# Optimization experiments

Hardware: AMD Instinct MI355X
Metric: run time of the kernel (lower is better)

## Reference

```python
import jax, jax.numpy as jnp
import numpy as np

N_GRAPHS = 8


def glorot(key, shape):
    fan_in, fan_out = shape[0], shape[1]
    s = (6.0 / (fan_in + fan_out)) ** 0.5
    return jax.random.uniform(key, shape, jnp.float32, -s, s)


def setup_inputs() -> dict:
    key = jax.random.key(0)
    ks = jax.random.split(key, 8)
    N, E, C = 100000, 800000, 128
    x = jax.random.normal(ks[0], (N, C), jnp.float32)
    edge_index = jax.random.randint(ks[1], (2, E), 0, N, jnp.int64)
    batch = jnp.sort(jax.random.randint(ks[2], (N,), 0, N_GRAPHS, jnp.int64))
    W1 = glorot(ks[3], (C, 64));   b1 = jnp.zeros((64,), jnp.float32)
    W2 = glorot(ks[4], (64, 128)); b2 = jnp.zeros((128,), jnp.float32)
    W3 = glorot(ks[5], (128, 256)); b3 = jnp.zeros((256,), jnp.float32)
    Wfc = glorot(ks[6], (256, 1))
    bfc = jax.random.normal(ks[7], (1,), jnp.float32) * 0.01
    return {"x": x, "edge_index": edge_index, "batch": batch,
            "W1": W1, "b1": b1, "W2": W2, "b2": b2, "W3": W3, "b3": b3,
            "Wfc": Wfc, "bfc": bfc}


def _gcn_layer(h_in, W, b, src, dst, norm_edge, self_coef, n):
    # GCNConv: x' = D^{-1/2}(A+I)D^{-1/2} (x W) + b   (self-loops included)
    h = h_in @ W                                     # [N, out]
    msg = h[src] * norm_edge[:, None]                # gather + edge normalize
    agg = jax.ops.segment_sum(msg, dst, num_segments=n)  # scatter-add
    agg = agg + h * self_coef[:, None]               # self-loop contribution
    return agg + b


def reference(x, edge_index, batch, W1, b1, W2, b2, W3, b3, Wfc, bfc):
    n = x.shape[0]
    src, dst = edge_index[0], edge_index[1]
    # gcn_norm with self-loops: deg = in-degree + 1
    deg = jax.ops.segment_sum(jnp.ones_like(dst, dtype=x.dtype), dst, num_segments=n) + 1.0
    dis = deg ** -0.5
    norm_edge = dis[src] * dis[dst]
    self_coef = dis * dis
    h = jax.nn.relu(_gcn_layer(x, W1, b1, src, dst, norm_edge, self_coef, n))
    h = jax.nn.relu(_gcn_layer(h, W2, b2, src, dst, norm_edge, self_coef, n))
    h = jax.nn.relu(_gcn_layer(h, W3, b3, src, dst, norm_edge, self_coef, n))
    # global_mean_pool over graphs
    counts = jax.ops.segment_sum(jnp.ones((n,), x.dtype), batch, num_segments=N_GRAPHS)
    pooled = jax.ops.segment_sum(h, batch, num_segments=N_GRAPHS) / counts[:, None]
    return pooled @ Wfc + bfc
```

## Files before the change

### kernel.cpp

```cpp
#include <hip/hip_runtime.h>
#include <hip/hip_bf16.h>

typedef __attribute__((ext_vector_type(8))) short short8v;
typedef __attribute__((ext_vector_type(4))) float f32x4;

static __device__ __forceinline__ unsigned short f2bf(float f) {
  __hip_bfloat16 b = __float2bfloat16(f);
  return *reinterpret_cast<unsigned short*>(&b);
}
static __device__ __forceinline__ float bf2f(unsigned short u) {
  unsigned int x = ((unsigned int)u) << 16;
  return __builtin_bit_cast(float, x);
}
static __device__ __forceinline__ float bflo(unsigned int u) {
  return __builtin_bit_cast(float, u << 16);
}
static __device__ __forceinline__ float bfhi(unsigned int u) {
  return __builtin_bit_cast(float, u & 0xffff0000u);
}

__global__ __launch_bounds__(256) void k_hist(const int* __restrict__ ei,
                                              int* __restrict__ cnt, int E) {
  int stride = gridDim.x * blockDim.x;
  for (int i = blockIdx.x * blockDim.x + threadIdx.x; i < E; i += stride)
    atomicAdd(&cnt[ei[E + i]], 1);
}

__global__ __launch_bounds__(256) void k_scan1(const int* __restrict__ cnt,
                                               int* __restrict__ row_tmp,
                                               int* __restrict__ bsum, int N) {
  __shared__ int sd[256];
  const int tid = threadIdx.x;
  const int i = blockIdx.x * 256 + tid;
  int v = (i < N) ? cnt[i] : 0;
  sd[tid] = v;
  __syncthreads();
#pragma unroll
  for (int off = 1; off < 256; off <<= 1) {
    int t = (tid >= off) ? sd[tid - off] : 0;
    __syncthreads();
    sd[tid] += t;
    __syncthreads();
  }
  if (i < N) row_tmp[i] = sd[tid] - v;
  if (tid == 255) bsum[blockIdx.x] = sd[255];
}

__global__ __launch_bounds__(1024) void k_scan2(int* __restrict__ bsum, int nb) {
  __shared__ int sd[1024];
  const int t = threadIdx.x;
  int v = (t < nb) ? bsum[t] : 0;
  sd[t] = v;
  __syncthreads();
#pragma unroll
  for (int off = 1; off < 1024; off <<= 1) {
    int x = (t >= off) ? sd[t - off] : 0;
    __syncthreads();
    sd[t] += x;
    __syncthreads();
  }
  if (t < nb) bsum[t] = sd[t] - v;
}

__global__ __launch_bounds__(256) void k_scan3(const int* __restrict__ row_tmp,
                                               const int* __restrict__ bsum,
                                               const int* __restrict__ cnt,
                                               const int* __restrict__ batch,
                                               float* __restrict__ dis,
                                               int* __restrict__ row_ptr,
                                               int* __restrict__ bucket_cur,
                                               int* __restrict__ gstart, int N,
                                               int E) {
  const int i = blockIdx.x * 256 + threadIdx.x;
  if (i < N) {
    int rp = row_tmp[i] + bsum[i >> 8];
    row_ptr[i] = rp;
    if ((i & 255) == 0) bucket_cur[i >> 8] = rp;
    dis[i] = 1.0f / sqrtf((float)cnt[i] + 1.0f);
    int b = batch[i];
    if (i == 0) {
      for (int g = 0; g <= b; ++g) gstart[g] = 0;
    } else {
      int p = batch[i - 1];
      for (int g = p + 1; g <= b; ++g) gstart[g] = i;
    }
    if (i == N - 1)
      for (int g = b + 1; g <= 8; ++g) gstart[g] = N;
  }
  if (i == 0) row_ptr[N] = E;
}

__global__ __launch_bounds__(256) void k_b3(const int* __restrict__ ei,
                                            int* __restrict__ bucket_cur,
                                            uint2* __restrict__ pairs, int E) {
  __shared__ int cntD[512];
  __shared__ int gbase[512];
  const int t = threadIdx.x;
  for (int i = t; i < 512; i += 256) cntD[i] = 0;
  __syncthreads();
  const int base = blockIdx.x * 2048;
  int s[8], d[8], rk[8];
#pragma unroll
  for (int i = 0; i < 8; ++i) {
    int e = base + i * 256 + t;
    if (e < E) {
      s[i] = ei[e];
      d[i] = ei[E + e];
      rk[i] = atomicAdd(&cntD[d[i] >> 8], 1);
    }
  }
  __syncthreads();
  for (int i = t; i < 512; i += 256)
    if (cntD[i] > 0) gbase[i] = atomicAdd(&bucket_cur[i], cntD[i]);
  __syncthreads();
#pragma unroll
  for (int i = 0; i < 8; ++i) {
    int e = base + i * 256 + t;
    if (e < E)
      pairs[gbase[d[i] >> 8] + rk[i]] = make_uint2((unsigned)s[i], (unsigned)d[i]);
  }
}

__global__ __launch_bounds__(256) void k_b4(const int* __restrict__ row_ptr,
                                            const uint2* __restrict__ pairs,
                                            int* __restrict__ col, int N) {
  __shared__ int curL[257];
  const int n0 = blockIdx.x << 8;
  const int nn = min(256, N - n0);
  const int t = threadIdx.x;
  for (int i = t; i <= nn; i += 256) curL[i] = row_ptr[n0 + i];
  __syncthreads();
  const int p0 = curL[0], p1 = curL[nn];
  __syncthreads();
  for (int idx = p0 + t; idx < p1; idx += 256) {
    uint2 pr = pairs[idx];
    int pos = atomicAdd(&curL[(int)pr.y - n0], 1);
    col[pos] = (int)pr.x;
  }
}

static __device__ __forceinline__ void pack_one(const float* __restrict__ W,
                                                unsigned short* __restrict__ Wp,
                                                int K, int M, int t) {
  int KT = K >> 5;
  int lane = t & 63;
  int tile = t >> 6;
  int kt = tile % KT;
  int ct = tile / KT;
  int c = ct * 16 + (lane & 15);
  int k0 = kt * 32 + (lane >> 4) * 8;
  unsigned short v[8];
#pragma unroll
  for (int j = 0; j < 8; ++j) v[j] = f2bf(W[(size_t)(k0 + j) * M + c]);
  ushort4* dst = (ushort4*)&Wp[(size_t)t * 8];
  dst[0] = make_ushort4(v[0], v[1], v[2], v[3]);
  dst[1] = make_ushort4(v[4], v[5], v[6], v[7]);
}

__global__ __launch_bounds__(256) void k_packall(
    const float* __restrict__ W1, const float* __restrict__ W2,
    const float* __restrict__ W3, unsigned short* __restrict__ Wp1,
    unsigned short* __restrict__ Wp2, unsigned short* __restrict__ Wp3) {
  int t = blockIdx.x * 256 + threadIdx.x;
  if (t < 1024)
    pack_one(W1, Wp1, 128, 64, t);
  else if (t < 2048)
    pack_one(W2, Wp2, 64, 128, t - 1024);
  else if (t < 6144)
    pack_one(W3, Wp3, 128, 256, t - 2048);
}

template <bool EPI>
__global__ __launch_bounds__(256) void k_agg64(const int* __restrict__ row_ptr,
                                               const int* __restrict__ col,
                                               const float* __restrict__ dis,
                                               const unsigned short* __restrict__ Hin,
                                               const float* __restrict__ bias,
                                               unsigned short* __restrict__ Pout,
                                               int N) {
  const int lane = threadIdx.x & 63;
  int d = blockIdx.x * 4 + (threadIdx.x >> 6);
  if (d >= N) return;
  const int q = lane >> 3;
  const int cl = lane & 7;
  const int cb = cl * 8;
  const float disd = dis[d];
  const int beg = row_ptr[d];
  const int end = row_ptr[d + 1];
  const int deg = end - beg;
  const int nedge = min(deg, 64);

  int s_l = d;
  float w_l = 0.f;
  if (lane < nedge) {
    s_l = col[beg + lane];
    w_l = dis[s_l] * disd;
  }

  float acc[8];
#pragma unroll
  for (int k = 0; k < 8; ++k) acc[k] = 0.f;
  if (q == 0) {
    uint4 u = *(const uint4*)&Hin[(size_t)d * 64 + cb];
    const float sc = disd * disd;
    acc[0] = bflo(u.x) * sc; acc[1] = bfhi(u.x) * sc;
    acc[2] = bflo(u.y) * sc; acc[3] = bfhi(u.y) * sc;
    acc[4] = bflo(u.z) * sc; acc[5] = bfhi(u.z) * sc;
    acc[6] = bflo(u.w) * sc; acc[7] = bfhi(u.w) * sc;
  }

  const int padded = (nedge + 15) & ~15;
  for (int base = 0; base < padded; base += 16) {
    int e0 = base + q, e1 = base + 8 + q;
    int s0 = __shfl(s_l, e0, 64);
    float w0 = __shfl(w_l, e0, 64);
    int s1 = __shfl(s_l, e1, 64);
    float w1 = __shfl(w_l, e1, 64);
    if (e0 >= nedge) { s0 = d; w0 = 0.f; }
    if (e1 >= nedge) { s1 = d; w1 = 0.f; }
    uint4 u0 = *(const uint4*)&Hin[(size_t)s0 * 64 + cb];
    uint4 u1 = *(const uint4*)&Hin[(size_t)s1 * 64 + cb];
    acc[0] = fmaf(bflo(u0.x), w0, acc[0]); acc[1] = fmaf(bfhi(u0.x), w0, acc[1]);
    acc[2] = fmaf(bflo(u0.y), w0, acc[2]); acc[3] = fmaf(bfhi(u0.y), w0, acc[3]);
    acc[4] = fmaf(bflo(u0.z), w0, acc[4]); acc[5] = fmaf(bfhi(u0.z), w0, acc[5]);
    acc[6] = fmaf(bflo(u0.w), w0, acc[6]); acc[7] = fmaf(bfhi(u0.w), w0, acc[7]);
    acc[0] = fmaf(bflo(u1.x), w1, acc[0]); acc[1] = fmaf(bfhi(u1.x), w1, acc[1]);
    acc[2] = fmaf(bflo(u1.y), w1, acc[2]); acc[3] = fmaf(bfhi(u1.y), w1, acc[3]);
    acc[4] = fmaf(bflo(u1.z), w1, acc[4]); acc[5] = fmaf(bfhi(u1.z), w1, acc[5]);
    acc[6] = fmaf(bflo(u1.w), w1, acc[6]); acc[7] = fmaf(bfhi(u1.w), w1, acc[7]);
  }
  if (deg > 64) {
    for (int j = beg + 64 + q; j < end; j += 8) {
      int s = col[j];
      float w = dis[s] * disd;
      uint4 u = *(const uint4*)&Hin[(size_t)s * 64 + cb];
      acc[0] = fmaf(bflo(u.x), w, acc[0]); acc[1] = fmaf(bfhi(u.x), w, acc[1]);
      acc[2] = fmaf(bflo(u.y), w, acc[2]); acc[3] = fmaf(bfhi(u.y), w, acc[3]);
      acc[4] = fmaf(bflo(u.z), w, acc[4]); acc[5] = fmaf(bfhi(u.z), w, acc[5]);
      acc[6] = fmaf(bflo(u.w), w, acc[6]); acc[7] = fmaf(bfhi(u.w), w, acc[7]);
    }
  }

#pragma unroll
  for (int k = 0; k < 8; ++k) {
    acc[k] += __shfl_xor(acc[k], 8, 64);
    acc[k] += __shfl_xor(acc[k], 16, 64);
    acc[k] += __shfl_xor(acc[k], 32, 64);
  }
  if (q == 0) {
    if (EPI) {
#pragma unroll
      for (int k = 0; k < 8; ++k) acc[k] = fmaxf(acc[k] + bias[cb + k], 0.f);
    }
    uint4 o;
    o.x = (unsigned)f2bf(acc[0]) | ((unsigned)f2bf(acc[1]) << 16);
    o.y = (unsigned)f2bf(acc[2]) | ((unsigned)f2bf(acc[3]) << 16);
    o.z = (unsigned)f2bf(acc[4]) | ((unsigned)f2bf(acc[5]) << 16);
    o.w = (unsigned)f2bf(acc[6]) | ((unsigned)f2bf(acc[7]) << 16);
    *(uint4*)&Pout[(size_t)d * 64 + cb] = o;
  }
}

__global__ __launch_bounds__(256) void k_agg128(const int* __restrict__ row_ptr,
                                                const int* __restrict__ col,
                                                const float* __restrict__ dis,
                                                const unsigned short* __restrict__ Hin,
                                                unsigned short* __restrict__ Pout,
                                                int N) {
  const int lane = threadIdx.x & 63;
  int d = blockIdx.x * 4 + (threadIdx.x >> 6);
  if (d >= N) return;
  const int q = lane >> 4;
  const int cl = lane & 15;
  const int cb = cl * 8;
  const float disd = dis[d];
  const int beg = row_ptr[d];
  const int end = row_ptr[d + 1];
  const int deg = end - beg;
  const int nedge = min(deg, 64);

  int s_l = d;
  float w_l = 0.f;
  if (lane < nedge) {
    s_l = col[beg + lane];
    w_l = dis[s_l] * disd;
  }

  float acc[8];
#pragma unroll
  for (int k = 0; k < 8; ++k) acc[k] = 0.f;
  if (q == 0) {
    uint4 u = *(const uint4*)&Hin[(size_t)d * 128 + cb];
    const float sc = disd * disd;
    acc[0] = bflo(u.x) * sc; acc[1] = bfhi(u.x) * sc;
    acc[2] = bflo(u.y) * sc; acc[3] = bfhi(u.y) * sc;
    acc[4] = bflo(u.z) * sc; acc[5] = bfhi(u.z) * sc;
    acc[6] = bflo(u.w) * sc; acc[7] = bfhi(u.w) * sc;
  }

  const int padded = (nedge + 7) & ~7;
  for (int base = 0; base < padded; base += 8) {
    int e0 = base + q, e1 = base + 4 + q;
    int s0 = __shfl(s_l, e0, 64);
    float w0 = __shfl(w_l, e0, 64);
    int s1 = __shfl(s_l, e1, 64);
    float w1 = __shfl(w_l, e1, 64);
    if (e0 >= nedge) { s0 = d; w0 = 0.f; }
    if (e1 >= nedge) { s1 = d; w1 = 0.f; }
    uint4 u0 = *(const uint4*)&Hin[(size_t)s0 * 128 + cb];
    uint4 u1 = *(const uint4*)&Hin[(size_t)s1 * 128 + cb];
    acc[0] = fmaf(bflo(u0.x), w0, acc[0]); acc[1] = fmaf(bfhi(u0.x), w0, acc[1]);
    acc[2] = fmaf(bflo(u0.y), w0, acc[2]); acc[3] = fmaf(bfhi(u0.y), w0, acc[3]);
    acc[4] = fmaf(bflo(u0.z), w0, acc[4]); acc[5] = fmaf(bfhi(u0.z), w0, acc[5]);
    acc[6] = fmaf(bflo(u0.w), w0, acc[6]); acc[7] = fmaf(bfhi(u0.w), w0, acc[7]);
    acc[0] = fmaf(bflo(u1.x), w1, acc[0]); acc[1] = fmaf(bfhi(u1.x), w1, acc[1]);
    acc[2] = fmaf(bflo(u1.y), w1, acc[2]); acc[3] = fmaf(bfhi(u1.y), w1, acc[3]);
    acc[4] = fmaf(bflo(u1.z), w1, acc[4]); acc[5] = fmaf(bfhi(u1.z), w1, acc[5]);
    acc[6] = fmaf(bflo(u1.w), w1, acc[6]); acc[7] = fmaf(bfhi(u1.w), w1, acc[7]);
  }
  if (deg > 64) {
    for (int j = beg + 64 + q; j < end; j += 4) {
      int s = col[j];
      float w = dis[s] * disd;
      uint4 u = *(const uint4*)&Hin[(size_t)s * 128 + cb];
      acc[0] = fmaf(bflo(u.x), w, acc[0]); acc[1] = fmaf(bfhi(u.x), w, acc[1]);
      acc[2] = fmaf(bflo(u.y), w, acc[2]); acc[3] = fmaf(bfhi(u.y), w, acc[3]);
      acc[4] = fmaf(bflo(u.z), w, acc[4]); acc[5] = fmaf(bfhi(u.z), w, acc[5]);
      acc[6] = fmaf(bflo(u.w), w, acc[6]); acc[7] = fmaf(bfhi(u.w), w, acc[7]);
    }
  }

#pragma unroll
  for (int k = 0; k < 8; ++k) {
    acc[k] += __shfl_xor(acc[k], 16, 64);
    acc[k] += __shfl_xor(acc[k], 32, 64);
  }
  if (q == 0) {
    uint4 o;
    o.x = (unsigned)f2bf(acc[0]) | ((unsigned)f2bf(acc[1]) << 16);
    o.y = (unsigned)f2bf(acc[2]) | ((unsigned)f2bf(acc[3]) << 16);
    o.z = (unsigned)f2bf(acc[4]) | ((unsigned)f2bf(acc[5]) << 16);
    o.w = (unsigned)f2bf(acc[6]) | ((unsigned)f2bf(acc[7]) << 16);
    *(uint4*)&Pout[(size_t)d * 128 + cb] = o;
  }
}

template <int K, int M, bool F32IN, bool BIAS>
__global__ __launch_bounds__(256) void k_mmx(const void* __restrict__ Ap,
                                             const unsigned short* __restrict__ Wp,
                                             const float* __restrict__ bias,
                                             unsigned short* __restrict__ Hout,
                                             int N) {
  constexpr int KT = K / 32, CTW = M / 64;
  __shared__ unsigned short lds[64][M + 8];
  const int lane = threadIdx.x & 63;
  const int wid = threadIdx.x >> 6;
  const int blk0 = blockIdx.x * 64;
  const int r = lane & 15;
  const int kh = lane >> 4;

  int ar[4];
#pragma unroll
  for (int rt = 0; rt < 4; ++rt) ar[rt] = min(blk0 + rt * 16 + r, N - 1);

  f32x4 acc[4][CTW];
#pragma unroll
  for (int rt = 0; rt < 4; ++rt)
#pragma unroll
    for (int c = 0; c < CTW; ++c) acc[rt][c] = (f32x4){0.f, 0.f, 0.f, 0.f};

#pragma unroll
  for (int kt = 0; kt < KT; ++kt) {
    short8v a[4];
#pragma unroll
    for (int rt = 0; rt < 4; ++rt) {
      if (F32IN) {
        const float* Af = (const float*)Ap;
        const float* p = &Af[(size_t)ar[rt] * K + kt * 32 + kh * 8];
        float4 f0 = *(const float4*)p;
        float4 f1 = *(const float4*)(p + 4);
        a[rt][0] = (short)f2bf(f0.x); a[rt][1] = (short)f2bf(f0.y);
        a[rt][2] = (short)f2bf(f0.z); a[rt][3] = (short)f2bf(f0.w);
        a[rt][4] = (short)f2bf(f1.x); a[rt][5] = (short)f2bf(f1.y);
        a[rt][6] = (short)f2bf(f1.z); a[rt][7] = (short)f2bf(f1.w);
      } else {
        const unsigned short* Ab = (const unsigned short*)Ap;
        a[rt] = *(const short8v*)&Ab[(size_t)ar[rt] * K + kt * 32 + kh * 8];
      }
    }
#pragma unroll
    for (int c = 0; c < CTW; ++c) {
      const int ct = wid * CTW + c;
      short8v b = *(const short8v*)&Wp[(size_t)((ct * KT + kt) * 64 + lane) * 8];
#pragma unroll
      for (int rt = 0; rt < 4; ++rt)
        acc[rt][c] = __builtin_amdgcn_mfma_f32_16x16x32_bf16(a[rt], b, acc[rt][c], 0, 0, 0);
    }
  }

#pragma unroll
  for (int c = 0; c < CTW; ++c) {
    const int col = (wid * CTW + c) * 16 + r;
    const float bv = BIAS ? bias[col] : 0.f;
#pragma unroll
    for (int rt = 0; rt < 4; ++rt) {
      const int lrow0 = rt * 16 + kh * 4;
#pragma unroll
      for (int reg = 0; reg < 4; ++reg) {
        float v = acc[rt][c][reg] + bv;
        if (BIAS) v = fmaxf(v, 0.f);
        lds[lrow0 + reg][col] = f2bf(v);
      }
    }
  }
  __syncthreads();
  constexpr int CBK = M / 8;
  constexpr int ITER = 64 * CBK / 256;
  const int t = threadIdx.x;
#pragma unroll
  for (int it = 0; it < ITER; ++it) {
    int idx = it * 256 + t;
    int row = idx / CBK;
    int cbk = idx % CBK;
    if (blk0 + row < N)
      *(uint4*)&Hout[(size_t)(blk0 + row) * M + cbk * 8] =
          *(const uint4*)&lds[row][cbk * 8];
  }
}

__global__ __launch_bounds__(256) void k_pool2(const unsigned short* __restrict__ H4,
                                               const int* __restrict__ gstart,
                                               float* __restrict__ pooled) {
  __shared__ float sd[8][256];
  const int g = blockIdx.y;
  const int s = gstart[g], e = gstart[g + 1];
  if (s >= e) return;
  const int PB = gridDim.x;
  const int chunk = (e - s + PB - 1) / PB;
  const int r0 = s + blockIdx.x * chunk;
  const int r1 = min(e, r0 + chunk);

  const int t = threadIdx.x;
  const int rs = t >> 5;
  const int cl = t & 31;
  const int cb = cl * 8;

  float a[8];
#pragma unroll
  for (int k = 0; k < 8; ++k) a[k] = 0.f;

  for (int r = r0 + rs; r < r1; r += 8) {
    uint4 u = *(const uint4*)&H4[(size_t)r * 256 + cb];
    a[0] += bflo(u.x); a[1] += bfhi(u.x);
    a[2] += bflo(u.y); a[3] += bfhi(u.y);
    a[4] += bflo(u.z); a[5] += bfhi(u.z);
    a[6] += bflo(u.w); a[7] += bfhi(u.w);
  }
#pragma unroll
  for (int k = 0; k < 8; ++k) sd[rs][cb + k] = a[k];
  __syncthreads();
  float v = 0.f;
#pragma unroll
  for (int q = 0; q < 8; ++q) v += sd[q][t];
  atomicAdd(&pooled[g * 256 + t], v);
}

__global__ __launch_bounds__(256) void k_final(const float* __restrict__ pooled,
                                               const int* __restrict__ gstart,
                                               const float* __restrict__ Wfc,
                                               const float* __restrict__ bfc,
                                               float* __restrict__ out) {
  __shared__ float red[4];
  const int t = threadIdx.x;
  for (int g = 0; g < 8; ++g) {
    float cg = (float)(gstart[g + 1] - gstart[g]);
    float v = pooled[g * 256 + t] / cg * Wfc[t];
#pragma unroll
    for (int off = 32; off > 0; off >>= 1) v += __shfl_down(v, off, 64);
    if ((t & 63) == 0) red[t >> 6] = v;
    __syncthreads();
    if (t == 0) out[g] = red[0] + red[1] + red[2] + red[3] + bfc[0];
    __syncthreads();
  }
}

extern "C" void kernel_launch(void* const* d_in, const int* in_sizes, int n_in,
                              void* d_out, int out_size, void* d_ws,
                              size_t ws_size, hipStream_t stream) {
  const float* x = (const float*)d_in[0];
  const int* ei = (const int*)d_in[1];
  const int* batch = (const int*)d_in[2];
  const float* W1 = (const float*)d_in[3];
  const float* b1 = (const float*)d_in[4];
  const float* W2 = (const float*)d_in[5];
  const float* b2 = (const float*)d_in[6];
  const float* W3 = (const float*)d_in[7];
  const float* b3 = (const float*)d_in[8];
  const float* Wfc = (const float*)d_in[9];
  const float* bfc = (const float*)d_in[10];
  float* out = (float*)d_out;

  const int N = in_sizes[0] / 128;
  const int E = in_sizes[1] / 2;
  const int nb = (N + 255) / 256;
  const int nbk = (N + 255) >> 8;

  float* ws = (float*)d_ws;
  size_t o = 0;
  float* dis = ws + o;            o += (size_t)N;
  int* cnt = (int*)(ws + o);      o += (size_t)N;
  int* row_tmp = (int*)(ws + o);  o += (size_t)N;
  int* bsum = (int*)(ws + o);     o += 1024;
  int* row_ptr = (int*)(ws + o);  o += (size_t)N + 1;
  int* bucket_cur = (int*)(ws + o); o += 512;
  int* col = (int*)(ws + o);      o += (size_t)E;
  uint2* pairs = (uint2*)(ws + o); o += (size_t)E * 2;
  float* pooled = ws + o;         o += 2048;
  int* gstart = (int*)(ws + o);   o += 16;
  unsigned short* Wp1 = (unsigned short*)(ws + o); o += 4096;
  unsigned short* Wp2 = (unsigned short*)(ws + o); o += 4096;
  unsigned short* Wp3 = (unsigned short*)(ws + o); o += 16384;
  o = (o + 63) & ~(size_t)63;
  unsigned short* bufA = (unsigned short*)(ws + o); o += (size_t)N * 32;
  unsigned short* bufB = (unsigned short*)(ws + o); o += (size_t)N * 32;
  unsigned short* bufC = (unsigned short*)(ws + o); o += (size_t)N * 64;
  unsigned short* bufD = (unsigned short*)(ws + o); o += (size_t)N * 64;
  unsigned short* bufE = (unsigned short*)(ws + o); o += (size_t)N * 128;

  hipMemsetAsync(cnt, 0, (size_t)N * sizeof(int), stream);
  hipMemsetAsync(pooled, 0, 2048 * sizeof(float), stream);

  k_hist<<<2048, 256, 0, stream>>>(ei, cnt, E);
  k_scan1<<<nb, 256, 0, stream>>>(cnt, row_tmp, bsum, N);
  k_scan2<<<1, 1024, 0, stream>>>(bsum, nb);
  k_scan3<<<nb, 256, 0, stream>>>(row_tmp, bsum, cnt, batch, dis, row_ptr,
                                  bucket_cur, gstart, N, E);
  k_b3<<<(E + 2047) / 2048, 256, 0, stream>>>(ei, bucket_cur, pairs, E);
  k_b4<<<nbk, 256, 0, stream>>>(row_ptr, pairs, col, N);
  k_packall<<<24, 256, 0, stream>>>(W1, W2, W3, Wp1, Wp2, Wp3);

  const int ablocks = (N + 3) / 4;
  const int mblocks = (N + 63) / 64;
  k_mmx<128, 64, true, false><<<mblocks, 256, 0, stream>>>(x, Wp1, nullptr, bufA, N);
  k_agg64<true><<<ablocks, 256, 0, stream>>>(row_ptr, col, dis, bufA, b1, bufB, N);
  k_agg64<false><<<ablocks, 256, 0, stream>>>(row_ptr, col, dis, bufB, nullptr, bufA, N);
  k_mmx<64, 128, false, true><<<mblocks, 256, 0, stream>>>(bufA, Wp2, b2, bufC, N);
  k_agg128<<<ablocks, 256, 0, stream>>>(row_ptr, col, dis, bufC, bufD, N);
  k_mmx<128, 256, false, true><<<mblocks, 256, 0, stream>>>(bufD, Wp3, b3, bufE, N);

  k_pool2<<<dim3(128, 8), 256, 0, stream>>>(bufE, gstart, pooled);
  k_final<<<1, 256, 0, stream>>>(pooled, gstart, Wfc, bfc, out);
}
```

Before: 385.5 us.

## Build CSR via bucket histogram and per-bucket local scan instead of global scan

Replaces the per-node global degree histogram and three-kernel scan with a 256-node bucket histogram done in shared memory, a single-block scan over 512 buckets, and a per-bucket kernel that counts degrees locally, scans them, and writes row_ptr and dis before scattering col. This removes the N-sized memset, the global per-node atomics and two launches, but reads the pairs array twice in the final kernel. The batch graph-start computation moves into its own small kernel, and the two memsets are merged into one.

```diff
diff --git a/kernel.cpp b/kernel.cpp
--- a/kernel.cpp
+++ b/kernel.cpp
@@ -19,79 +19,43 @@
   return __builtin_bit_cast(float, u & 0xffff0000u);
 }
 
-__global__ __launch_bounds__(256) void k_hist(const int* __restrict__ ei,
-                                              int* __restrict__ cnt, int E) {
+__global__ __launch_bounds__(256) void k_bhist(const int* __restrict__ ei,
+                                               int* __restrict__ bcnt, int E) {
+  __shared__ int h[512];
+  const int t = threadIdx.x;
+  for (int i = t; i < 512; i += 256) h[i] = 0;
+  __syncthreads();
   int stride = gridDim.x * blockDim.x;
-  for (int i = blockIdx.x * blockDim.x + threadIdx.x; i < E; i += stride)
-    atomicAdd(&cnt[ei[E + i]], 1);
-}
-
-__global__ __launch_bounds__(256) void k_scan1(const int* __restrict__ cnt,
-                                               int* __restrict__ row_tmp,
-                                               int* __restrict__ bsum, int N) {
-  __shared__ int sd[256];
-  const int tid = threadIdx.x;
-  const int i = blockIdx.x * 256 + tid;
-  int v = (i < N) ? cnt[i] : 0;
-  sd[tid] = v;
-  __syncthreads();
-#pragma unroll
-  for (int off = 1; off < 256; off <<= 1) {
-    int t = (tid >= off) ? sd[tid - off] : 0;
-    __syncthreads();
-    sd[tid] += t;
-    __syncthreads();
-  }
-  if (i < N) row_tmp[i] = sd[tid] - v;
-  if (tid == 255) bsum[blockIdx.x] = sd[255];
-}
-
-__global__ __launch_bounds__(1024) void k_scan2(int* __restrict__ bsum, int nb) {
-  __shared__ int sd[1024];
-  const int t = threadIdx.x;
-  int v = (t < nb) ? bsum[t] : 0;
+  for (int i = blockIdx.x * blockDim.x + t; i < E; i += stride)
+    atomicAdd(&h[ei[E + i] >> 8], 1);
+  __syncthreads();
+  for (int i = t; i < 512; i += 256)
+    if (h[i]) atomicAdd(&bcnt[i], h[i]);
+}
+
+__global__ __launch_bounds__(512) void k_bscan(const int* __restrict__ bcnt,
+                                               int* __restrict__ bbase,
+                                               int* __restrict__ bcur, int E) {
+  __shared__ int sd[512];
+  const int t = threadIdx.x;
+  int v = bcnt[t];
   sd[t] = v;
   __syncthreads();
 #pragma unroll
-  for (int off = 1; off < 1024; off <<= 1) {
+  for (int off = 1; off < 512; off <<= 1) {
     int x = (t >= off) ? sd[t - off] : 0;
     __syncthreads();
     sd[t] += x;
     __syncthreads();
   }
-  if (t < nb) bsum[t] = sd[t] - v;
-}
-
-__global__ __launch_bounds__(256) void k_scan3(const int* __restrict__ row_tmp,
-                                               const int* __restrict__ bsum,
-                                               const int* __restrict__ cnt,
-                                               const int* __restrict__ batch,
-                                               float* __restrict__ dis,
-                                               int* __restrict__ row_ptr,
-                                               int* __restrict__ bucket_cur,
-                                               int* __restrict__ gstart, int N,
-                                               int E) {
-  const int i = blockIdx.x * 256 + threadIdx.x;
-  if (i < N) {
-    int rp = row_tmp[i] + bsum[i >> 8];
-    row_ptr[i] = rp;
-    if ((i & 255) == 0) bucket_cur[i >> 8] = rp;
-    dis[i] = 1.0f / sqrtf((float)cnt[i] + 1.0f);
-    int b = batch[i];
-    if (i == 0) {
-      for (int g = 0; g <= b; ++g) gstart[g] = 0;
-    } else {
-      int p = batch[i - 1];
-      for (int g = p + 1; g <= b; ++g) gstart[g] = i;
-    }
-    if (i == N - 1)
-      for (int g = b + 1; g <= 8; ++g) gstart[g] = N;
-  }
-  if (i == 0) row_ptr[N] = E;
+  int ex = sd[t] - v;
+  bbase[t] = ex;
+  bcur[t] = ex;
+  if (t == 511) bbase[512] = sd[511];
 }
 
 __global__ __launch_bounds__(256) void k_b3(const int* __restrict__ ei,
-                                            int* __restrict__ bucket_cur,
+                                            int* __restrict__ bcur,
                                             uint2* __restrict__ pairs, int E) {
   __shared__ int cntD[512];
   __shared__ int gbase[512];
@@ -111,7 +75,7 @@
   }
   __syncthreads();
   for (int i = t; i < 512; i += 256)
-    if (cntD[i] > 0) gbase[i] = atomicAdd(&bucket_cur[i], cntD[i]);
+    if (cntD[i] > 0) gbase[i] = atomicAdd(&bcur[i], cntD[i]);
   __syncthreads();
 #pragma unroll
   for (int i = 0; i < 8; ++i) {
@@ -121,22 +85,62 @@
   }
 }
 
-__global__ __launch_bounds__(256) void k_b4(const int* __restrict__ row_ptr,
-                                            const uint2* __restrict__ pairs,
-                                            int* __restrict__ col, int N) {
-  __shared__ int curL[257];
+__global__ __launch_bounds__(256) void k_b4x(const int* __restrict__ bbase,
+                                             const uint2* __restrict__ pairs,
+                                             int* __restrict__ col,
+                                             int* __restrict__ row_ptr,
+                                             float* __restrict__ dis, int N,
+                                             int E) {
+  __shared__ int cntL[256];
+  __shared__ int sd[256];
+  __shared__ int curL[256];
   const int n0 = blockIdx.x << 8;
   const int nn = min(256, N - n0);
   const int t = threadIdx.x;
-  for (int i = t; i <= nn; i += 256) curL[i] = row_ptr[n0 + i];
-  __syncthreads();
-  const int p0 = curL[0], p1 = curL[nn];
+  cntL[t] = 0;
+  __syncthreads();
+  const int p0 = bbase[blockIdx.x], p1 = bbase[blockIdx.x + 1];
+  for (int idx = p0 + t; idx < p1; idx += 256)
+    atomicAdd(&cntL[(int)pairs[idx].y - n0], 1);
+  __syncthreads();
+  const int c = cntL[t];
+  sd[t] = c;
+  __syncthreads();
+#pragma unroll
+  for (int off = 1; off < 256; off <<= 1) {
+    int x = (t >= off) ? sd[t - off] : 0;
+    __syncthreads();
+    sd[t] += x;
+    __syncthreads();
+  }
+  const int excl = sd[t] - c;
+  if (t < nn) {
+    row_ptr[n0 + t] = p0 + excl;
+    dis[n0 + t] = 1.0f / sqrtf((float)c + 1.0f);
+  }
+  curL[t] = p0 + excl;
+  if (blockIdx.x == gridDim.x - 1 && t == 0) row_ptr[N] = E;
   __syncthreads();
   for (int idx = p0 + t; idx < p1; idx += 256) {
     uint2 pr = pairs[idx];
     int pos = atomicAdd(&curL[(int)pr.y - n0], 1);
     col[pos] = (int)pr.x;
   }
+}
+
+__global__ __launch_bounds__(256) void k_gb(const int* __restrict__ batch,
+                                            int* __restrict__ gstart, int N) {
+  const int i = blockIdx.x * 256 + threadIdx.x;
+  if (i >= N) return;
+  int b = batch[i];
+  if (i == 0) {
+    for (int g = 0; g <= b; ++g) gstart[g] = 0;
+  } else {
+    int p = batch[i - 1];
+    for (int g = p + 1; g <= b; ++g) gstart[g] = i;
+  }
+  if (i == N - 1)
+    for (int g = b + 1; g <= 8; ++g) gstart[g] = N;
 }
 
 static __device__ __forceinline__ void pack_one(const float* __restrict__ W,
@@ -508,14 +512,13 @@
   float* ws = (float*)d_ws;
   size_t o = 0;
   float* dis = ws + o;            o += (size_t)N;
-  int* cnt = (int*)(ws + o);      o += (size_t)N;
-  int* row_tmp = (int*)(ws + o);  o += (size_t)N;
-  int* bsum = (int*)(ws + o);     o += 1024;
   int* row_ptr = (int*)(ws + o);  o += (size_t)N + 1;
-  int* bucket_cur = (int*)(ws + o); o += 512;
+  int* bcnt = (int*)(ws + o);     o += 512;
+  float* pooled = ws + o;         o += 2048;
+  int* bbase = (int*)(ws + o);    o += 513;
+  int* bcur = (int*)(ws + o);     o += 512;
   int* col = (int*)(ws + o);      o += (size_t)E;
   uint2* pairs = (uint2*)(ws + o); o += (size_t)E * 2;
-  float* pooled = ws + o;         o += 2048;
   int* gstart = (int*)(ws + o);   o += 16;
   unsigned short* Wp1 = (unsigned short*)(ws + o); o += 4096;
   unsigned short* Wp2 = (unsigned short*)(ws + o); o += 4096;
@@ -527,16 +530,13 @@
   unsigned short* bufD = (unsigned short*)(ws + o); o += (size_t)N * 64;
   unsigned short* bufE = (unsigned short*)(ws + o); o += (size_t)N * 128;
 
-  hipMemsetAsync(cnt, 0, (size_t)N * sizeof(int), stream);
-  hipMemsetAsync(pooled, 0, 2048 * sizeof(float), stream);
-
-  k_hist<<<2048, 256, 0, stream>>>(ei, cnt, E);
-  k_scan1<<<nb, 256, 0, stream>>>(cnt, row_tmp, bsum, N);
-  k_scan2<<<1, 1024, 0, stream>>>(bsum, nb);
-  k_scan3<<<nb, 256, 0, stream>>>(row_tmp, bsum, cnt, batch, dis, row_ptr,
-                                  bucket_cur, gstart, N, E);
-  k_b3<<<(E + 2047) / 2048, 256, 0, stream>>>(ei, bucket_cur, pairs, E);
-  k_b4<<<nbk, 256, 0, stream>>>(row_ptr, pairs, col, N);
+  hipMemsetAsync(bcnt, 0, (512 + 2048) * sizeof(float), stream);
+
+  k_bhist<<<512, 256, 0, stream>>>(ei, bcnt, E);
+  k_bscan<<<1, 512, 0, stream>>>(bcnt, bbase, bcur, E);
+  k_b3<<<(E + 2047) / 2048, 256, 0, stream>>>(ei, bcur, pairs, E);
+  k_b4x<<<nbk, 256, 0, stream>>>(bbase, pairs, col, row_ptr, dis, N, E);
+  k_gb<<<nb, 256, 0, stream>>>(batch, gstart, N);
   k_packall<<<24, 256, 0, stream>>>(W1, W2, W3, Wp1, Wp2, Wp3);
 
   const int ablocks = (N + 3) / 4;
```

Result: faster. 362.8 us (-5.9%).
